# Kernel optimization log

Measured on AMD Instinct MI355X. Metric: run time of the kernel, lower is better.

The kernel has to match this reference:

```python
import jax, jax.numpy as jnp
import numpy as np

EPS = 1e-10


def setup_inputs() -> dict:
    key = jax.random.key(0)
    k1, k2, k3 = jax.random.split(key, 3)
    B, L, D, C = 8, 1024, 1024, 8192
    mlc_emb = jax.random.normal(k1, (B, L, D), dtype=jnp.float32)
    embedding = jax.random.normal(k2, (C, D), dtype=jnp.float32)
    gumbel_u = jax.random.uniform(k3, (B, L, C), dtype=jnp.float32, minval=EPS, maxval=1.0)
    tau = jnp.float32(1.0)
    return {"mlc_emb": mlc_emb, "embedding": embedding, "gumbel_u": gumbel_u, "tau": tau}


def reference(mlc_emb, embedding, gumbel_u, tau):
    # logits = mlc_emb @ codebook^T : [B, L, C]
    logits = jnp.einsum('bld,cd->blc', mlc_emb, embedding)
    # gumbel-softmax (soft): g = -log(-log(u)); softmax((logits + g) / tau)
    gumbels = -jnp.log(-jnp.log(jnp.clip(gumbel_u, EPS, 1.0)))
    soft_one_hot = jax.nn.softmax((logits + gumbels) / tau, axis=-1)
    # quantized = soft weights @ codebook : [B, L, D]
    quantized = jnp.einsum('blc,cd->bld', soft_one_hot, embedding)
    codes = jnp.argmax(soft_one_hot, axis=-1)
    return quantized, codes
```

## Files before the change

### kernel.cpp

```cpp
#include <hip/hip_runtime.h>
#include <hip/hip_bf16.h>


#define M_ROWS 8192
#define C_COLS 8192
#define K_DIM  1024
#define CAND_CAP 512
#define CUT 16.0f
#define ABS_THR 70.0f
#define RESCORE_WIN 4.0f

typedef __bf16 bf16;
typedef bf16 bf16x8 __attribute__((ext_vector_type(8)));
typedef bf16 bf16x4 __attribute__((ext_vector_type(4)));
typedef float f32x4 __attribute__((ext_vector_type(4)));

__device__ __forceinline__ void gload_lds16(const bf16* g, bf16* l) {
  __builtin_amdgcn_global_load_lds(
      (const __attribute__((address_space(1))) unsigned int*)g,
      (__attribute__((address_space(3))) unsigned int*)l, 16, 0, 0);
}

__global__ __launch_bounds__(256) void split_kernel(
    const float4* __restrict__ src, bf16x4* __restrict__ hi,
    bf16x4* __restrict__ lo, int n4) {
  int i = blockIdx.x * blockDim.x + threadIdx.x;
  if (i >= n4) return;
  float4 v = src[i];
  float vv[4] = {v.x, v.y, v.z, v.w};
  bf16x4 h, l;
#pragma unroll
  for (int j = 0; j < 4; ++j) {
    bf16 hb = (bf16)vv[j];
    h[j] = hb;
    l[j] = (bf16)(vv[j] - (float)hb);
  }
  hi[i] = h;
  lo[i] = l;
}

__global__ __launch_bounds__(256, 2) void gemm_fused(
    const bf16* __restrict__ Ah, const bf16* __restrict__ Al,
    const bf16* __restrict__ Bh, const bf16* __restrict__ Bl,
    const float* __restrict__ gu, const float* __restrict__ tau,
    float* __restrict__ pmax, float* __restrict__ pden,
    int* __restrict__ cnt, float* __restrict__ cand_s, int* __restrict__ cand_i) {
  __shared__ __attribute__((aligned(16))) bf16 sAh[128 * 32];
  __shared__ __attribute__((aligned(16))) bf16 sAl[128 * 32];
  __shared__ __attribute__((aligned(16))) bf16 sBh[128 * 32];
  __shared__ __attribute__((aligned(16))) bf16 sBl[128 * 32];

  const int t = threadIdx.x;
  const int wave = t >> 6, lane = t & 63;
  const int wr = wave >> 1, wc = wave & 1;
  const int lg = lane >> 4, li = lane & 15;
  const int rowTile = blockIdx.y * 128;
  const int colTile = blockIdx.x * 128;

  f32x4 acc[4][4] = {};

  const int srow = t >> 2;
  const int skq = t & 3;
  const size_t aBase = (size_t)(rowTile + srow) * K_DIM + skq * 8;
  const size_t bBase = (size_t)(colTile + srow) * K_DIM + skq * 8;
  const int ldsOff = srow * 32 + skq * 8;

  for (int kt = 0; kt < K_DIM / 32; ++kt) {
    const size_t ko = (size_t)kt * 32;
    gload_lds16(&Ah[aBase + ko], &sAh[ldsOff]);
    gload_lds16(&Ah[aBase + ko + (size_t)64 * K_DIM], &sAh[ldsOff + 64 * 32]);
    gload_lds16(&Al[aBase + ko], &sAl[ldsOff]);
    gload_lds16(&Al[aBase + ko + (size_t)64 * K_DIM], &sAl[ldsOff + 64 * 32]);
    gload_lds16(&Bh[bBase + ko], &sBh[ldsOff]);
    gload_lds16(&Bh[bBase + ko + (size_t)64 * K_DIM], &sBh[ldsOff + 64 * 32]);
    gload_lds16(&Bl[bBase + ko], &sBl[ldsOff]);
    gload_lds16(&Bl[bBase + ko + (size_t)64 * K_DIM], &sBl[ldsOff + 64 * 32]);
    __syncthreads();

    bf16x8 fah[4], fal[4], fbh[4], fbl[4];
#pragma unroll
    for (int x = 0; x < 4; ++x) {
      const int ar = (wr * 64 + x * 16 + li) * 32 + lg * 8;
      const int br = (wc * 64 + x * 16 + li) * 32 + lg * 8;
      fah[x] = *(const bf16x8*)&sAh[ar];
      fal[x] = *(const bf16x8*)&sAl[ar];
      fbh[x] = *(const bf16x8*)&sBh[br];
      fbl[x] = *(const bf16x8*)&sBl[br];
    }
#pragma unroll
    for (int m = 0; m < 4; ++m)
#pragma unroll
      for (int n = 0; n < 4; ++n) {
        acc[m][n] = __builtin_amdgcn_mfma_f32_16x16x32_bf16(fah[m], fbh[n], acc[m][n], 0, 0, 0);
        acc[m][n] = __builtin_amdgcn_mfma_f32_16x16x32_bf16(fah[m], fbl[n], acc[m][n], 0, 0, 0);
        acc[m][n] = __builtin_amdgcn_mfma_f32_16x16x32_bf16(fal[m], fbh[n], acc[m][n], 0, 0, 0);
      }
    __syncthreads();
  }

  const float rtau = 1.0f / tau[0];
  const int chunk = (colTile >> 6) + wc;
#pragma unroll
  for (int m = 0; m < 4; ++m) {
#pragma unroll
    for (int j = 0; j < 4; ++j) {
      const int row = rowTile + wr * 64 + m * 16 + lg * 4 + j;
      float v[4];
#pragma unroll
      for (int n = 0; n < 4; ++n) {
        const int col = colTile + wc * 64 + n * 16 + li;
        float u = gu[(size_t)row * C_COLS + col];
        u = fminf(fmaxf(u, 1e-10f), 1.0f);
        const float gmb = -__logf(-logf(u));
        v[n] = (acc[m][n][j] + gmb) * rtau;
      }
      float mx = fmaxf(fmaxf(v[0], v[1]), fmaxf(v[2], v[3]));
#pragma unroll
      for (int msk = 1; msk < 16; msk <<= 1) mx = fmaxf(mx, __shfl_xor(mx, msk));
      float se = 0.f;
#pragma unroll
      for (int n = 0; n < 4; ++n) se += __expf(v[n] - mx);
#pragma unroll
      for (int msk = 1; msk < 16; msk <<= 1) se += __shfl_xor(se, msk);
      if (li == 0) {
        pmax[(size_t)row * 128 + chunk] = mx;
        pden[(size_t)row * 128 + chunk] = se;
      }
#pragma unroll
      for (int n = 0; n < 4; ++n) {
        const bool isChunkMax = (v[n] == mx);
        if ((v[n] >= mx - CUT && v[n] >= ABS_THR) || isChunkMax) {
          const int col = colTile + wc * 64 + n * 16 + li;
          const int slot = atomicAdd(&cnt[row], 1);
          if (slot < CAND_CAP) {
            cand_s[(size_t)row * CAND_CAP + slot] = v[n];
            cand_i[(size_t)row * CAND_CAP + slot] = col;
          }
        }
      }
    }
  }
}

__global__ __launch_bounds__(256) void finalize_kernel(
    const float* __restrict__ pmax, const float* __restrict__ pden,
    const int* __restrict__ cnt, const float* __restrict__ cand_s,
    const int* __restrict__ cand_i, const float* __restrict__ A,
    const float* __restrict__ emb, const float* __restrict__ gu,
    const float* __restrict__ tau, float* __restrict__ outq,
    float* __restrict__ outc) {
  const int row = blockIdx.x;
  const int t = threadIdx.x;
  __shared__ float sred[256];
  __shared__ int sidx[256];
  __shared__ float csc[64];
  __shared__ int cid[64];
  __shared__ int ncontrib;

  sred[t] = (t < 128) ? pmax[(size_t)row * 128 + t] : -INFINITY;
  __syncthreads();
  for (int s = 128; s > 0; s >>= 1) {
    if (t < s) sred[t] = fmaxf(sred[t], sred[t + s]);
    __syncthreads();
  }
  const float gmax = sred[0];
  __syncthreads();
  sred[t] = (t < 128)
                ? pden[(size_t)row * 128 + t] * __expf(pmax[(size_t)row * 128 + t] - gmax)
                : 0.f;
  __syncthreads();
  for (int s = 128; s > 0; s >>= 1) {
    if (t < s) sred[t] += sred[t + s];
    __syncthreads();
  }
  const float den = sred[0];
  __syncthreads();

  if (t == 0) ncontrib = 0;
  __syncthreads();

  int n = cnt[row];
  if (n > CAND_CAP) n = CAND_CAP;
  for (int k = t; k < n; k += 256) {
    const float s_ = cand_s[(size_t)row * CAND_CAP + k];
    if (s_ >= gmax - CUT) {
      const int slot = atomicAdd(&ncontrib, 1);
      if (slot < 64) {
        csc[slot] = s_;
        cid[slot] = cand_i[(size_t)row * CAND_CAP + k];
      }
    }
  }
  __syncthreads();
  int nc = ncontrib;
  if (nc > 64) nc = 64;

  const float rtau = 1.0f / tau[0];
  const float* ar = A + (size_t)row * K_DIM;
  for (int k = 0; k < nc; ++k) {
    if (csc[k] < gmax - RESCORE_WIN) continue;
    const float* er = emb + (size_t)cid[k] * K_DIM;
    float p = ar[t] * er[t] + ar[t + 256] * er[t + 256] + ar[t + 512] * er[t + 512] +
              ar[t + 768] * er[t + 768];
    sred[t] = p;
    __syncthreads();
    for (int s = 128; s > 0; s >>= 1) {
      if (t < s) sred[t] += sred[t + s];
      __syncthreads();
    }
    if (t == 0) {
      float u = gu[(size_t)row * C_COLS + cid[k]];
      u = fminf(fmaxf(u, 1e-10f), 1.0f);
      const float gmb = -__logf(-logf(u));
      csc[k] = (sred[0] + gmb) * rtau;
    }
    __syncthreads();
  }

  float bs = -INFINITY;
  int bi = 0x7FFFFFFF;
  for (int k = t; k < nc; k += 256) {
    const float s_ = csc[k];
    const int i_ = cid[k];
    if (s_ > bs || (s_ == bs && i_ < bi)) { bs = s_; bi = i_; }
  }
  sred[t] = bs;
  sidx[t] = bi;
  __syncthreads();
  for (int s = 128; s > 0; s >>= 1) {
    if (t < s) {
      if (sred[t + s] > sred[t] || (sred[t + s] == sred[t] && sidx[t + s] < sidx[t])) {
        sred[t] = sred[t + s];
        sidx[t] = sidx[t + s];
      }
    }
    __syncthreads();
  }

  float a0 = 0.f, a1 = 0.f, a2 = 0.f, a3 = 0.f;
  for (int k = 0; k < nc; ++k) {
    const float w = __expf(csc[k] - gmax) / den;
    const float* er = emb + (size_t)cid[k] * K_DIM;
    a0 += w * er[t];
    a1 += w * er[t + 256];
    a2 += w * er[t + 512];
    a3 += w * er[t + 768];
  }
  const size_t ob = (size_t)row * K_DIM;
  outq[ob + t] = a0;
  outq[ob + t + 256] = a1;
  outq[ob + t + 512] = a2;
  outq[ob + t + 768] = a3;
  if (t == 0) outc[row] = (float)sidx[0];
}

extern "C" void kernel_launch(void* const* d_in, const int* in_sizes, int n_in,
                              void* d_out, int out_size, void* d_ws, size_t ws_size,
                              hipStream_t stream) {
  const float* A = (const float*)d_in[0];
  const float* B = (const float*)d_in[1];
  const float* GU = (const float*)d_in[2];
  const float* TAU = (const float*)d_in[3];
  float* out = (float*)d_out;

  char* ws = (char*)d_ws;
  const size_t planeElems = (size_t)M_ROWS * K_DIM;
  bf16* Ah = (bf16*)ws; ws += planeElems * 2;
  bf16* Al = (bf16*)ws; ws += planeElems * 2;
  bf16* Bh = (bf16*)ws; ws += planeElems * 2;
  bf16* Bl = (bf16*)ws; ws += planeElems * 2;
  float* pmax = (float*)ws; ws += (size_t)M_ROWS * 128 * 4;
  float* pden = (float*)ws; ws += (size_t)M_ROWS * 128 * 4;
  int* cntp = (int*)ws; ws += (size_t)M_ROWS * 4;
  float* cs = (float*)ws; ws += (size_t)M_ROWS * CAND_CAP * 4;
  int* cip = (int*)ws; ws += (size_t)M_ROWS * CAND_CAP * 4;

  hipMemsetAsync(cntp, 0, M_ROWS * sizeof(int), stream);
  const int n4 = (int)(planeElems / 4);
  split_kernel<<<dim3((n4 + 255) / 256), 256, 0, stream>>>((const float4*)A, (bf16x4*)Ah,
                                                           (bf16x4*)Al, n4);
  split_kernel<<<dim3((n4 + 255) / 256), 256, 0, stream>>>((const float4*)B, (bf16x4*)Bh,
                                                           (bf16x4*)Bl, n4);
  gemm_fused<<<dim3(64, 64), 256, 0, stream>>>(Ah, Al, Bh, Bl, GU, TAU, pmax, pden, cntp, cs, cip);
  finalize_kernel<<<dim3(M_ROWS), 256, 0, stream>>>(pmax, pden, cntp, cs, cip, A, B, GU, TAU,
                                                    out, out + (size_t)M_ROWS * K_DIM);
}
```

Before: 1.058 ms.

## Double-buffer LDS tiles, swizzle block order, and stream gumbel loads nontemporally

Doubles the shared-memory buffers so the global-to-LDS loads for the next K tile are issued before the MFMA work on the current tile, cutting the number of barriers per iteration from two to one. Block indices are remapped so consecutive blocks cover 32-column stripes of the codebook across all row tiles, which is meant to improve L2 reuse of B. Gumbel noise reads use nontemporal loads to avoid polluting the cache. LDS use doubles to 64KB per block, which may limit occupancy under the 2-blocks-per-SM launch bound.

Result: slower. 1.102 ms (+4.2%).

```diff
diff --git a/kernel.cpp b/kernel.cpp
--- a/kernel.cpp
+++ b/kernel.cpp
@@ -45,17 +45,21 @@
     const float* __restrict__ gu, const float* __restrict__ tau,
     float* __restrict__ pmax, float* __restrict__ pden,
     int* __restrict__ cnt, float* __restrict__ cand_s, int* __restrict__ cand_i) {
-  __shared__ __attribute__((aligned(16))) bf16 sAh[128 * 32];
-  __shared__ __attribute__((aligned(16))) bf16 sAl[128 * 32];
-  __shared__ __attribute__((aligned(16))) bf16 sBh[128 * 32];
-  __shared__ __attribute__((aligned(16))) bf16 sBl[128 * 32];
+  __shared__ __attribute__((aligned(16))) bf16 sAh[2][128 * 32];
+  __shared__ __attribute__((aligned(16))) bf16 sAl[2][128 * 32];
+  __shared__ __attribute__((aligned(16))) bf16 sBh[2][128 * 32];
+  __shared__ __attribute__((aligned(16))) bf16 sBl[2][128 * 32];
 
   const int t = threadIdx.x;
   const int wave = t >> 6, lane = t & 63;
   const int wr = wave >> 1, wc = wave & 1;
   const int lg = lane >> 4, li = lane & 15;
-  const int rowTile = blockIdx.y * 128;
-  const int colTile = blockIdx.x * 128;
+
+  const int bid = blockIdx.y * gridDim.x + blockIdx.x;
+  const int str = bid >> 11;
+  const int w_ = bid & 2047;
+  const int rowTile = (w_ >> 5) * 128;
+  const int colTile = ((str << 5) + (w_ & 31)) * 128;
 
   f32x4 acc[4][4] = {};
 
@@ -65,27 +69,28 @@
   const size_t bBase = (size_t)(colTile + srow) * K_DIM + skq * 8;
   const int ldsOff = srow * 32 + skq * 8;
 
-  for (int kt = 0; kt < K_DIM / 32; ++kt) {
+  auto stage = [&](int buf, int kt) {
     const size_t ko = (size_t)kt * 32;
-    gload_lds16(&Ah[aBase + ko], &sAh[ldsOff]);
-    gload_lds16(&Ah[aBase + ko + (size_t)64 * K_DIM], &sAh[ldsOff + 64 * 32]);
-    gload_lds16(&Al[aBase + ko], &sAl[ldsOff]);
-    gload_lds16(&Al[aBase + ko + (size_t)64 * K_DIM], &sAl[ldsOff + 64 * 32]);
-    gload_lds16(&Bh[bBase + ko], &sBh[ldsOff]);
-    gload_lds16(&Bh[bBase + ko + (size_t)64 * K_DIM], &sBh[ldsOff + 64 * 32]);
-    gload_lds16(&Bl[bBase + ko], &sBl[ldsOff]);
-    gload_lds16(&Bl[bBase + ko + (size_t)64 * K_DIM], &sBl[ldsOff + 64 * 32]);
-    __syncthreads();
-
+    gload_lds16(&Ah[aBase + ko], &sAh[buf][ldsOff]);
+    gload_lds16(&Ah[aBase + ko + (size_t)64 * K_DIM], &sAh[buf][ldsOff + 64 * 32]);
+    gload_lds16(&Al[aBase + ko], &sAl[buf][ldsOff]);
+    gload_lds16(&Al[aBase + ko + (size_t)64 * K_DIM], &sAl[buf][ldsOff + 64 * 32]);
+    gload_lds16(&Bh[bBase + ko], &sBh[buf][ldsOff]);
+    gload_lds16(&Bh[bBase + ko + (size_t)64 * K_DIM], &sBh[buf][ldsOff + 64 * 32]);
+    gload_lds16(&Bl[bBase + ko], &sBl[buf][ldsOff]);
+    gload_lds16(&Bl[bBase + ko + (size_t)64 * K_DIM], &sBl[buf][ldsOff + 64 * 32]);
+  };
+
+  auto compute = [&](int buf) {
     bf16x8 fah[4], fal[4], fbh[4], fbl[4];
 #pragma unroll
     for (int x = 0; x < 4; ++x) {
       const int ar = (wr * 64 + x * 16 + li) * 32 + lg * 8;
       const int br = (wc * 64 + x * 16 + li) * 32 + lg * 8;
-      fah[x] = *(const bf16x8*)&sAh[ar];
-      fal[x] = *(const bf16x8*)&sAl[ar];
-      fbh[x] = *(const bf16x8*)&sBh[br];
-      fbl[x] = *(const bf16x8*)&sBl[br];
+      fah[x] = *(const bf16x8*)&sAh[buf][ar];
+      fal[x] = *(const bf16x8*)&sAl[buf][ar];
+      fbh[x] = *(const bf16x8*)&sBh[buf][br];
+      fbl[x] = *(const bf16x8*)&sBl[buf][br];
     }
 #pragma unroll
     for (int m = 0; m < 4; ++m)
@@ -95,8 +100,16 @@
         acc[m][n] = __builtin_amdgcn_mfma_f32_16x16x32_bf16(fah[m], fbl[n], acc[m][n], 0, 0, 0);
         acc[m][n] = __builtin_amdgcn_mfma_f32_16x16x32_bf16(fal[m], fbh[n], acc[m][n], 0, 0, 0);
       }
-    __syncthreads();
-  }
+  };
+
+  stage(0, 0);
+  __syncthreads();
+  for (int kt = 0; kt < K_DIM / 32 - 1; ++kt) {
+    stage((kt + 1) & 1, kt + 1);
+    compute(kt & 1);
+    __syncthreads();
+  }
+  compute((K_DIM / 32 - 1) & 1);
 
   const float rtau = 1.0f / tau[0];
   const int chunk = (colTile >> 6) + wc;
@@ -109,7 +122,7 @@
 #pragma unroll
       for (int n = 0; n < 4; ++n) {
         const int col = colTile + wc * 64 + n * 16 + li;
-        float u = gu[(size_t)row * C_COLS + col];
+        float u = __builtin_nontemporal_load(&gu[(size_t)row * C_COLS + col]);
         u = fminf(fmaxf(u, 1e-10f), 1.0f);
         const float gmb = -__logf(-logf(u));
         v[n] = (acc[m][n][j] + gmb) * rtau;
```
